# Optimization experiments

Hardware: AMD Instinct MI355X
Metric: run time of the kernel (lower is better)

Reference implementation:

```python
import jax, jax.numpy as jnp
import numpy as np

B, T, D, H = 4, 2048, 1024, 16
DH = D // H
SCALE = 1.0 / np.sqrt(DH)


def setup_inputs() -> dict:
    key = jax.random.key(0)
    ks = jax.random.split(key, 8)
    s = 1.0 / np.sqrt(D)  # keep projections well-scaled
    return {
        "query": jax.random.normal(ks[0], (B, T, D), jnp.float32),
        "key": jax.random.normal(ks[1], (B, T, D), jnp.float32),
        "value": jax.random.normal(ks[2], (B, T, D), jnp.float32),
        "Wq": jax.random.normal(ks[3], (D, D), jnp.float32) * s,
        "bq": jnp.zeros((D,), jnp.float32),
        "Wk": jax.random.normal(ks[4], (D, D), jnp.float32) * s,
        "bk": jnp.zeros((D,), jnp.float32),
        "Wv": jax.random.normal(ks[5], (D, D), jnp.float32) * s,
        "bv": jnp.zeros((D,), jnp.float32),
        "Wo": jax.random.normal(ks[6], (D, D), jnp.float32) * s,
        "bo": jnp.zeros((D,), jnp.float32),
    }


def reference(query, key, value, Wq, bq, Wk, bk, Wv, bv, Wo, bo):
    # Linear projections (torch Linear: x @ W.T + b; W here stored as [out,in])
    Q = query @ Wq.T + bq            # [B,T,D]
    K = key @ Wk.T + bk
    V = value @ Wv.T + bv
    # split heads -> [B,H,T,DH]
    Q = Q.reshape(B, T, H, DH).transpose(0, 2, 1, 3)
    K = K.reshape(B, T, H, DH).transpose(0, 2, 1, 3)
    V = V.reshape(B, T, H, DH).transpose(0, 2, 1, 3)
    # scaled dot-product attention (chunking in the original is a memory
    # optimization, not a math change; no mask, eval-mode dropout = identity)
    scores = jnp.einsum("bhqd,bhkd->bhqk", Q, K) * SCALE
    attn = jax.nn.softmax(scores, axis=-1)
    out = jnp.einsum("bhqk,bhkd->bhqd", attn, V)  # [B,H,T,DH]
    out = out.transpose(0, 2, 1, 3).reshape(B, T, D)
    return out @ Wo.T + bo
```

## Files before the change

### kernel.cpp

```cpp
#include <hip/hip_runtime.h>
#include <hip/hip_bf16.h>

typedef __bf16 bf16x8 __attribute__((ext_vector_type(8)));
typedef float f32x4 __attribute__((ext_vector_type(4)));
typedef float f32x16 __attribute__((ext_vector_type(16)));
typedef unsigned int uint;
typedef unsigned short u16;

#define DEV static __device__ __forceinline__

DEV u16 f2bf(float x) {
    uint u = __builtin_bit_cast(uint, x);
    u += 0x7FFFu + ((u >> 16) & 1u);
    return (u16)(u >> 16);
}

DEV uint cvtpk(float lo, float hi) {
    uint r;
    asm("v_cvt_pk_bf16_f32 %0, %1, %2" : "=v"(r) : "v"(lo), "v"(hi));
    return r;
}

DEV void plswap(uint& a, uint& b) {
    asm("v_permlane32_swap_b32 %0, %1" : "+v"(a), "+v"(b));
}

DEV float fexp2(float x) { return __builtin_amdgcn_exp2f(x); }

DEV void gload16(const void* g, void* l) {
    __builtin_amdgcn_global_load_lds((const __attribute__((address_space(1))) void*)g,
                                     (__attribute__((address_space(3))) void*)l,
                                     16, 0, 0);
}

__global__ __launch_bounds__(256) void k_wconv(const float* __restrict__ w0,
                                               const float* __restrict__ w1,
                                               const float* __restrict__ w2,
                                               const float* __restrict__ w3,
                                               u16* __restrict__ out) {
    const int which = blockIdx.x >> 9;
    const float* in = which == 0 ? w0 : (which == 1 ? w1 : (which == 2 ? w2 : w3));
    const long i = (blockIdx.x & 511) * 256 + threadIdx.x;
    const float4* p = (const float4*)in + i * 2;
    float4 a = p[0], b = p[1];
    uint4 dv;
    dv.x = cvtpk(a.x, a.y); dv.y = cvtpk(a.z, a.w);
    dv.z = cvtpk(b.x, b.y); dv.w = cvtpk(b.z, b.w);
    ((uint4*)(out + ((long)which << 20)))[i] = dv;
}

__global__ __launch_bounds__(256, 2) void k_gemm_qkv(
    const float* __restrict__ Aq, const float* __restrict__ Ak,
    const float* __restrict__ Av, const u16* __restrict__ Bw,
    const float* __restrict__ b0, const float* __restrict__ b1,
    const float* __restrict__ b2, u16* __restrict__ Cb,
    u16* __restrict__ VT) {
    constexpr int N = 1024, K = 1024;
    __shared__ u16 lS[16384];
    u16* lA = lS;
    u16* lB = lS + 8192;
    const int tid = threadIdx.x;
    const int l = tid & 63, w = tid >> 6;
    const int lr = l & 15, lk = l >> 4;
    const int wr = w >> 1, wc = w & 1;
    const int nbn = N >> 7;
    const int cpx = (int)gridDim.x >> 3;
    const int wg = (blockIdx.x & 7) * cpx + (blockIdx.x >> 3);
    const int bm = wg / nbn, bn = wg % nbn;
    const int seg = bm >> 6;
    const float* Aseg = seg == 0 ? Aq : (seg == 1 ? Ak : Av);
    const u16* Bseg = Bw + ((long)seg << 20);
    const float* bias = seg == 0 ? b0 : (seg == 1 ? b1 : b2);
    const int bml = bm & 63;
    const float oscale = seg == 0 ? 0.18033688f : 1.0f;

    const int arow = tid >> 3;
    const int acol = (tid & 7) * 8;
    int adst[4];
    const float* asrc[4];
#pragma unroll
    for (int t = 0; t < 4; ++t) {
        int row = t * 32 + arow;
        adst[t] = row * 128 + ((acol * 2) ^ ((row & 7) << 4));
        asrc[t] = Aseg + (long)(bml * 128 + row) * K + acol;
    }
    long bbase[4];
    int bdst[4];
#pragma unroll
    for (int t = 0; t < 4; ++t) {
        int p = (t * 256 + tid) * 16;
        int row = p >> 7;
        int src = (p & 127) ^ ((row & 7) << 4);
        bdst[t] = p;
        bbase[t] = (long)(bn * 128 + row) * (K * 2) + src;
    }
    const int swz = (lr & 7) << 4;
    int aoff[4][2], boff[4][2];
#pragma unroll
    for (int m = 0; m < 4; ++m)
#pragma unroll
        for (int kc = 0; kc < 2; ++kc) {
            aoff[m][kc] = (wr * 64 + m * 16 + lr) * 128 + ((kc * 64 + lk * 16) ^ swz);
            boff[m][kc] = (wc * 64 + m * 16 + lr) * 128 + ((kc * 64 + lk * 16) ^ swz);
        }

    f32x4 acc[4][4] = {};
    const char* gB = (const char*)Bseg;
    const char* lAb = (const char*)lA;
    const char* lBb = (const char*)lB;
    for (int kt = 0; kt < K / 64; ++kt) {
        __syncthreads();
#pragma unroll
        for (int t = 0; t < 4; ++t)
            gload16(gB + bbase[t] + kt * 128, (char*)lB + bdst[t]);
        float4 f0[4], f1[4];
#pragma unroll
        for (int t = 0; t < 4; ++t) {
            const float* s = asrc[t] + kt * 64;
            f0[t] = *(const float4*)s;
            f1[t] = *(const float4*)(s + 4);
        }
#pragma unroll
        for (int t = 0; t < 4; ++t) {
            uint4 dv;
            dv.x = cvtpk(f0[t].x, f0[t].y);
            dv.y = cvtpk(f0[t].z, f0[t].w);
            dv.z = cvtpk(f1[t].x, f1[t].y);
            dv.w = cvtpk(f1[t].z, f1[t].w);
            *(uint4*)((char*)lA + adst[t]) = dv;
        }
        __syncthreads();
#pragma unroll
        for (int kc = 0; kc < 2; ++kc) {
            bf16x8 av[4], bv[4];
#pragma unroll
            for (int m = 0; m < 4; ++m) av[m] = *(const bf16x8*)(lAb + aoff[m][kc]);
#pragma unroll
            for (int n = 0; n < 4; ++n) bv[n] = *(const bf16x8*)(lBb + boff[n][kc]);
#pragma unroll
            for (int m = 0; m < 4; ++m)
#pragma unroll
                for (int n = 0; n < 4; ++n)
                    acc[m][n] = __builtin_amdgcn_mfma_f32_16x16x32_bf16(av[m], bv[n], acc[m][n], 0, 0, 0);
        }
    }

    const int col0 = bn * 128 + wc * 64;
    float bval[4];
#pragma unroll
    for (int n = 0; n < 4; ++n) bval[n] = bias[col0 + n * 16 + lr];

    if (seg < 2) {
        const int row0 = bm * 128 + wr * 64;
#pragma unroll
        for (int m = 0; m < 4; ++m)
#pragma unroll
            for (int j = 0; j < 4; ++j) {
                int row = row0 + m * 16 + lk * 4 + j;
#pragma unroll
                for (int n = 0; n < 4; ++n)
                    Cb[(long)row * N + col0 + n * 16 + lr] =
                        f2bf((acc[m][n][j] + bval[n]) * oscale);
            }
    } else {
        __syncthreads();
#pragma unroll
        for (int m = 0; m < 4; ++m)
#pragma unroll
            for (int j = 0; j < 4; ++j) {
                int row = wr * 64 + m * 16 + lk * 4 + j;
#pragma unroll
                for (int n = 0; n < 4; ++n) {
                    int col = wc * 64 + n * 16 + lr;
                    *(u16*)((char*)lS + col * 256 + ((row * 2) ^ ((col & 7) << 4))) =
                        f2bf(acc[m][n][j] + bval[n]);
                }
            }
        __syncthreads();
        const int bb = bml >> 4;
        const int t0 = (bml & 15) * 128;
        const int c = tid >> 4;
        const int chunk = tid & 15;
#pragma unroll
        for (int pass = 0; pass < 8; ++pass) {
            int cc = pass * 16 + c;
            uint4 val = *(const uint4*)((const char*)lS + cc * 256 +
                                        ((chunk * 16) ^ ((cc & 7) << 4)));
            int gcol = bn * 128 + cc;
            int hh = gcol >> 6, dh = gcol & 63;
            *(uint4*)((char*)VT +
                      ((((long)(bb * 16 + hh) * 64 + dh) << 11) + t0 + chunk * 8) * 2) = val;
        }
    }
}

__global__ __launch_bounds__(256, 2) void k_gemm_bt(
    const u16* __restrict__ A, const u16* __restrict__ Bw,
    const float* __restrict__ bias, float* __restrict__ Cf,
    int M, int N, int K) {
    __shared__ u16 lA[128 * 64];
    __shared__ u16 lB[128 * 64];
    const int tid = threadIdx.x;
    const int l = tid & 63, w = tid >> 6;
    const int lr = l & 15, lk = l >> 4;
    const int wr = w >> 1, wc = w & 1;
    const int nbn = N >> 7;
    const int cpx = (int)gridDim.x >> 3;
    const int wg = (blockIdx.x & 7) * cpx + (blockIdx.x >> 3);
    const int bm = wg / nbn, bn = wg % nbn;

    long abase[4], bbase[4];
    int ldst[4];
#pragma unroll
    for (int t = 0; t < 4; ++t) {
        int c = t * 256 + tid;
        int p = c * 16;
        int row = p >> 7;
        int inrow = p & 127;
        int src = inrow ^ ((row & 7) << 4);
        ldst[t] = p;
        abase[t] = (long)(bm * 128 + row) * (K * 2) + src;
        bbase[t] = (long)(bn * 128 + row) * (K * 2) + src;
    }
    const int swz = (lr & 7) << 4;
    int aoff[4][2], boff[4][2];
#pragma unroll
    for (int m = 0; m < 4; ++m)
#pragma unroll
        for (int kc = 0; kc < 2; ++kc) {
            aoff[m][kc] = (wr * 64 + m * 16 + lr) * 128 + ((kc * 64 + lk * 16) ^ swz);
            boff[m][kc] = (wc * 64 + m * 16 + lr) * 128 + ((kc * 64 + lk * 16) ^ swz);
        }

    f32x4 acc[4][4] = {};
    const char* gA = (const char*)A;
    const char* gB = (const char*)Bw;
    const char* lAb = (const char*)lA;
    const char* lBb = (const char*)lB;
    const int nkt = K >> 6;
    for (int kt = 0; kt < nkt; ++kt) {
        __syncthreads();
#pragma unroll
        for (int t = 0; t < 4; ++t)
            gload16(gA + abase[t] + kt * 128, (char*)lA + ldst[t]);
#pragma unroll
        for (int t = 0; t < 4; ++t)
            gload16(gB + bbase[t] + kt * 128, (char*)lB + ldst[t]);
        __syncthreads();
#pragma unroll
        for (int kc = 0; kc < 2; ++kc) {
            bf16x8 av[4], bv[4];
#pragma unroll
            for (int m = 0; m < 4; ++m) av[m] = *(const bf16x8*)(lAb + aoff[m][kc]);
#pragma unroll
            for (int n = 0; n < 4; ++n) bv[n] = *(const bf16x8*)(lBb + boff[n][kc]);
#pragma unroll
            for (int m = 0; m < 4; ++m)
#pragma unroll
                for (int n = 0; n < 4; ++n)
                    acc[m][n] = __builtin_amdgcn_mfma_f32_16x16x32_bf16(av[m], bv[n], acc[m][n], 0, 0, 0);
        }
    }

    const int row0 = bm * 128 + wr * 64;
    const int col0 = bn * 128 + wc * 64;
    float bval[4];
#pragma unroll
    for (int n = 0; n < 4; ++n) bval[n] = bias[col0 + n * 16 + lr];
#pragma unroll
    for (int m = 0; m < 4; ++m)
#pragma unroll
        for (int j = 0; j < 4; ++j) {
            int row = row0 + m * 16 + lk * 4 + j;
#pragma unroll
            for (int n = 0; n < 4; ++n)
                Cf[(long)row * N + col0 + n * 16 + lr] = acc[m][n][j] + bval[n];
        }
}

__global__ __launch_bounds__(512, 4) void k_attn6(
    const u16* __restrict__ Qb, const u16* __restrict__ Kb,
    const u16* __restrict__ VTb, u16* __restrict__ Ob) {
    constexpr int T = 2048, D = 1024;
    constexpr int NT = T / 64;
    __shared__ u16 sK[2][4096];
    __shared__ u16 sV[2][4096];
    const int tid = threadIdx.x;
    const int l = tid & 63, w = tid >> 6;
    const int hi = l >> 5;
    const int q32 = l & 31;
    const int hi16 = hi * 16;
    const int kswz = (q32 & 7) << 4;
    const int bid = blockIdx.x;
    const int bh = (bid & 7) * 8 + ((bid >> 3) & 7);
    const int qt = bid >> 6;
    const int b = bh >> 4, h = bh & 15;

    const char* Qg = (const char*)(Qb + (long)b * T * D + h * 64);
    const char* Kg = (const char*)(Kb + (long)b * T * D + h * 64);
    const char* VTg = (const char*)(VTb + (long)bh * 64 * 2048);
    const int q0 = qt * 256 + w * 32;

    bf16x8 qf[4];
#pragma unroll
    for (int c = 0; c < 4; ++c)
        qf[c] = *(const bf16x8*)(Qg + (long)(q0 + q32) * 2048 + c * 32 + hi16);

    const int srow = tid >> 3;
    const int ssrc = ((tid & 7) * 16) ^ ((srow & 7) << 4);
    const int sdst = tid * 16;
    const long kbase = (long)srow * 2048 + ssrc;
    const long vbase = (long)srow * 4096 + ssrc;

    union { u16 s[8]; bf16x8 v; } ones_u;
#pragma unroll
    for (int i = 0; i < 8; ++i) ones_u.s[i] = 0x3F80;
    const bf16x8 onesv = ones_u.v;

#define STAGE(kt_, buf_) do {                                                  \
        gload16(Kg + (long)(kt_) * 64 * 2048 + kbase, (char*)sK[buf_] + sdst); \
        gload16(VTg + (kt_) * 128 + vbase, (char*)sV[buf_] + sdst);            \
    } while (0)

    STAGE(0, 0);
    __syncthreads();

    f32x16 o[2] = {};
    f32x16 lacc = {};

    for (int kt = 0; kt < NT; ++kt) {
        if (kt + 1 < NT) STAGE(kt + 1, (kt + 1) & 1);

        const char* kbp = (const char*)sK[kt & 1];
        f32x16 st[2] = {};
        __builtin_amdgcn_s_setprio(1);
#pragma unroll
        for (int c = 0; c < 4; ++c) {
            bf16x8 kf = *(const bf16x8*)(kbp + q32 * 128 + ((c * 32 + hi16) ^ kswz));
            st[0] = __builtin_amdgcn_mfma_f32_32x32x16_bf16(kf, qf[c], st[0], 0, 0, 0);
        }
#pragma unroll
        for (int c = 0; c < 4; ++c) {
            bf16x8 kf = *(const bf16x8*)(kbp + (32 + q32) * 128 + ((c * 32 + hi16) ^ kswz));
            st[1] = __builtin_amdgcn_mfma_f32_32x32x16_bf16(kf, qf[c], st[1], 0, 0, 0);
        }
        __builtin_amdgcn_s_setprio(0);

#pragma unroll
        for (int n = 0; n < 2; ++n)
#pragma unroll
            for (int r = 0; r < 16; ++r)
                st[n][r] = fexp2(st[n][r]);

        const char* vbp = (const char*)sV[kt & 1];
        __builtin_amdgcn_s_setprio(1);
#pragma unroll
        for (int c = 0; c < 4; ++c) {
            const int n = c >> 1, rb = (c & 1) * 8;
            uint A0 = cvtpk(st[n][rb + 0], st[n][rb + 1]);
            uint A1 = cvtpk(st[n][rb + 2], st[n][rb + 3]);
            uint B0 = cvtpk(st[n][rb + 4], st[n][rb + 5]);
            uint B1 = cvtpk(st[n][rb + 6], st[n][rb + 7]);
            plswap(A0, B0);
            plswap(A1, B1);
            union { uint u[4]; bf16x8 v; } pa;
            pa.u[0] = A0; pa.u[1] = A1; pa.u[2] = B0; pa.u[3] = B1;
            int cb = c * 32 + hi16;
            bf16x8 v0 = *(const bf16x8*)(vbp + q32 * 128 + (cb ^ kswz));
            bf16x8 v1 = *(const bf16x8*)(vbp + (32 + q32) * 128 + (cb ^ kswz));
            o[0] = __builtin_amdgcn_mfma_f32_32x32x16_bf16(pa.v, v0, o[0], 0, 0, 0);
            o[1] = __builtin_amdgcn_mfma_f32_32x32x16_bf16(pa.v, v1, o[1], 0, 0, 0);
            lacc  = __builtin_amdgcn_mfma_f32_32x32x16_bf16(pa.v, onesv, lacc, 0, 0, 0);
        }
        __builtin_amdgcn_s_setprio(0);
        __syncthreads();
    }
#undef STAGE

#pragma unroll
    for (int r = 0; r < 16; ++r) {
        float inv = 1.f / lacc[r];
        int srcq = (r & 3) + 8 * (r >> 2) + 4 * hi;
        int trow = q0 + srcq;
        char* orow = (char*)Ob + ((long)(b * T + trow) * D + h * 64) * 2;
        *(u16*)(orow + q32 * 2) = f2bf(o[0][r] * inv);
        *(u16*)(orow + (32 + q32) * 2) = f2bf(o[1][r] * inv);
    }
}

extern "C" void kernel_launch(void* const* d_in, const int* in_sizes, int n_in,
                              void* d_out, int out_size, void* d_ws, size_t ws_size,
                              hipStream_t stream) {
    const float* q  = (const float*)d_in[0];
    const float* k  = (const float*)d_in[1];
    const float* v  = (const float*)d_in[2];
    const float* Wq = (const float*)d_in[3];
    const float* bq = (const float*)d_in[4];
    const float* Wk = (const float*)d_in[5];
    const float* bk = (const float*)d_in[6];
    const float* Wv = (const float*)d_in[7];
    const float* bv = (const float*)d_in[8];
    const float* Wo = (const float*)d_in[9];
    const float* bo = (const float*)d_in[10];

    const long MT = 8192L * 1024;
    const long WT = 1024L * 1024;
    u16* ws   = (u16*)d_ws;
    u16* wall = ws;
    u16* qbf  = wall + 4 * WT;
    u16* kbf  = qbf + MT;
    u16* vtb  = kbf + MT;
    u16* abf  = vtb + MT;

    k_wconv<<<dim3(2048), dim3(256), 0, stream>>>(Wq, Wk, Wv, Wo, wall);

    k_gemm_qkv<<<dim3(1536), dim3(256), 0, stream>>>(q, k, v, wall,
                                                     bq, bk, bv, qbf, vtb);

    k_attn6<<<dim3(512), dim3(512), 0, stream>>>(qbf, kbf, vtb, abf);

    k_gemm_bt<<<dim3(512), dim3(256), 0, stream>>>(abf, wall + 3 * WT, bo,
                                                   (float*)d_out, 8192, 1024, 1024);
}
```

Baseline: 188.2 us.

## Compute softmax row sums on VALU and stage 128-key tiles per iteration

The attention kernel now loads 128 keys and values per pipeline stage instead of 64 and processes them as two halves. This halves the number of barriers and stage issues per block. The softmax denominator is no longer accumulated with an extra MFMA against a ones vector; instead each lane sums its exponentials in fp32 registers and combines them across lanes with shuffles. This removes a third of the PV-phase MFMAs, but doubles shared memory per block (64 KB), which may reduce how many blocks fit per CU.

```diff
diff --git a/kernel.cpp b/kernel.cpp
--- a/kernel.cpp
+++ b/kernel.cpp
@@ -278,13 +278,13 @@
         }
 }
 
-__global__ __launch_bounds__(512, 4) void k_attn6(
+__global__ __launch_bounds__(512, 4) void k_attn7(
     const u16* __restrict__ Qb, const u16* __restrict__ Kb,
     const u16* __restrict__ VTb, u16* __restrict__ Ob) {
     constexpr int T = 2048, D = 1024;
-    constexpr int NT = T / 64;
-    __shared__ u16 sK[2][4096];
-    __shared__ u16 sV[2][4096];
+    constexpr int NT2 = T / 128;
+    __shared__ u16 sK[2][8192];
+    __shared__ u16 sV[2][8192];
     const int tid = threadIdx.x;
     const int l = tid & 63, w = tid >> 6;
     const int hi = l >> 5;
@@ -306,81 +306,97 @@
     for (int c = 0; c < 4; ++c)
         qf[c] = *(const bf16x8*)(Qg + (long)(q0 + q32) * 2048 + c * 32 + hi16);
 
-    const int srow = tid >> 3;
-    const int ssrc = ((tid & 7) * 16) ^ ((srow & 7) << 4);
-    const int sdst = tid * 16;
-    const long kbase = (long)srow * 2048 + ssrc;
-    const long vbase = (long)srow * 4096 + ssrc;
-
-    union { u16 s[8]; bf16x8 v; } ones_u;
-#pragma unroll
-    for (int i = 0; i < 8; ++i) ones_u.s[i] = 0x3F80;
-    const bf16x8 onesv = ones_u.v;
-
-#define STAGE(kt_, buf_) do {                                                  \
-        gload16(Kg + (long)(kt_) * 64 * 2048 + kbase, (char*)sK[buf_] + sdst); \
-        gload16(VTg + (kt_) * 128 + vbase, (char*)sV[buf_] + sdst);            \
+    long kbase[2], vbase[2];
+    int sdst[2];
+#pragma unroll
+    for (int t = 0; t < 2; ++t) {
+        int id = tid + t * 512;
+        sdst[t] = id * 16;
+        int kr = id >> 3, kp = (id & 7) * 16;
+        kbase[t] = (long)kr * 2048 + (kp ^ ((kr & 7) << 4));
+        int vr = id >> 4, vp = (id & 15) * 16;
+        vbase[t] = (long)vr * 4096 + (vp ^ ((vr & 7) << 4));
+    }
+
+#define STAGE2(kt_, buf_) do {                                                  \
+        long kb = (long)(kt_) * 128 * 2048;                                     \
+        gload16(Kg + kb + kbase[0], (char*)sK[buf_] + sdst[0]);                 \
+        gload16(Kg + kb + kbase[1], (char*)sK[buf_] + sdst[1]);                 \
+        gload16(VTg + (kt_) * 256 + vbase[0], (char*)sV[buf_] + sdst[0]);       \
+        gload16(VTg + (kt_) * 256 + vbase[1], (char*)sV[buf_] + sdst[1]);       \
     } while (0)
 
-    STAGE(0, 0);
+    STAGE2(0, 0);
     __syncthreads();
 
     f32x16 o[2] = {};
-    f32x16 lacc = {};
-
-    for (int kt = 0; kt < NT; ++kt) {
-        if (kt + 1 < NT) STAGE(kt + 1, (kt + 1) & 1);
+    float ls0 = 0.f, ls1 = 0.f, ls2 = 0.f, ls3 = 0.f;
+
+    for (int kt = 0; kt < NT2; ++kt) {
+        if (kt + 1 < NT2) STAGE2(kt + 1, (kt + 1) & 1);
 
         const char* kbp = (const char*)sK[kt & 1];
-        f32x16 st[2] = {};
-        __builtin_amdgcn_s_setprio(1);
-#pragma unroll
-        for (int c = 0; c < 4; ++c) {
-            bf16x8 kf = *(const bf16x8*)(kbp + q32 * 128 + ((c * 32 + hi16) ^ kswz));
-            st[0] = __builtin_amdgcn_mfma_f32_32x32x16_bf16(kf, qf[c], st[0], 0, 0, 0);
-        }
-#pragma unroll
-        for (int c = 0; c < 4; ++c) {
-            bf16x8 kf = *(const bf16x8*)(kbp + (32 + q32) * 128 + ((c * 32 + hi16) ^ kswz));
-            st[1] = __builtin_amdgcn_mfma_f32_32x32x16_bf16(kf, qf[c], st[1], 0, 0, 0);
-        }
-        __builtin_amdgcn_s_setprio(0);
-
-#pragma unroll
-        for (int n = 0; n < 2; ++n)
-#pragma unroll
-            for (int r = 0; r < 16; ++r)
-                st[n][r] = fexp2(st[n][r]);
-
         const char* vbp = (const char*)sV[kt & 1];
-        __builtin_amdgcn_s_setprio(1);
-#pragma unroll
-        for (int c = 0; c < 4; ++c) {
-            const int n = c >> 1, rb = (c & 1) * 8;
-            uint A0 = cvtpk(st[n][rb + 0], st[n][rb + 1]);
-            uint A1 = cvtpk(st[n][rb + 2], st[n][rb + 3]);
-            uint B0 = cvtpk(st[n][rb + 4], st[n][rb + 5]);
-            uint B1 = cvtpk(st[n][rb + 6], st[n][rb + 7]);
-            plswap(A0, B0);
-            plswap(A1, B1);
-            union { uint u[4]; bf16x8 v; } pa;
-            pa.u[0] = A0; pa.u[1] = A1; pa.u[2] = B0; pa.u[3] = B1;
-            int cb = c * 32 + hi16;
-            bf16x8 v0 = *(const bf16x8*)(vbp + q32 * 128 + (cb ^ kswz));
-            bf16x8 v1 = *(const bf16x8*)(vbp + (32 + q32) * 128 + (cb ^ kswz));
-            o[0] = __builtin_amdgcn_mfma_f32_32x32x16_bf16(pa.v, v0, o[0], 0, 0, 0);
-            o[1] = __builtin_amdgcn_mfma_f32_32x32x16_bf16(pa.v, v1, o[1], 0, 0, 0);
-            lacc  = __builtin_amdgcn_mfma_f32_32x32x16_bf16(pa.v, onesv, lacc, 0, 0, 0);
-        }
-        __builtin_amdgcn_s_setprio(0);
-        __syncthreads();
-    }
-#undef STAGE
-
+#pragma unroll
+        for (int half = 0; half < 2; ++half) {
+            f32x16 st[2] = {};
+            __builtin_amdgcn_s_setprio(1);
+#pragma unroll
+            for (int c = 0; c < 4; ++c) {
+                bf16x8 kf = *(const bf16x8*)(kbp + (half * 64 + q32) * 128 +
+                                             ((c * 32 + hi16) ^ kswz));
+                st[0] = __builtin_amdgcn_mfma_f32_32x32x16_bf16(kf, qf[c], st[0], 0, 0, 0);
+            }
+#pragma unroll
+            for (int c = 0; c < 4; ++c) {
+                bf16x8 kf = *(const bf16x8*)(kbp + (half * 64 + 32 + q32) * 128 +
+                                             ((c * 32 + hi16) ^ kswz));
+                st[1] = __builtin_amdgcn_mfma_f32_32x32x16_bf16(kf, qf[c], st[1], 0, 0, 0);
+            }
+            __builtin_amdgcn_s_setprio(0);
+
+#pragma unroll
+            for (int n = 0; n < 2; ++n)
+#pragma unroll
+                for (int r = 0; r < 16; ++r) {
+                    float p = fexp2(st[n][r]);
+                    st[n][r] = p;
+                    if ((r & 3) == 0) ls0 += p;
+                    else if ((r & 3) == 1) ls1 += p;
+                    else if ((r & 3) == 2) ls2 += p;
+                    else ls3 += p;
+                }
+
+            __builtin_amdgcn_s_setprio(1);
+#pragma unroll
+            for (int c = 0; c < 4; ++c) {
+                const int n = c >> 1, rb = (c & 1) * 8;
+                uint A0 = cvtpk(st[n][rb + 0], st[n][rb + 1]);
+                uint A1 = cvtpk(st[n][rb + 2], st[n][rb + 3]);
+                uint B0 = cvtpk(st[n][rb + 4], st[n][rb + 5]);
+                uint B1 = cvtpk(st[n][rb + 6], st[n][rb + 7]);
+                plswap(A0, B0);
+                plswap(A1, B1);
+                union { uint u[4]; bf16x8 v; } pa;
+                pa.u[0] = A0; pa.u[1] = A1; pa.u[2] = B0; pa.u[3] = B1;
+                int cb = (c * 32 + hi16) ^ kswz;
+                bf16x8 v0 = *(const bf16x8*)(vbp + q32 * 256 + half * 128 + cb);
+                bf16x8 v1 = *(const bf16x8*)(vbp + (32 + q32) * 256 + half * 128 + cb);
+                o[0] = __builtin_amdgcn_mfma_f32_32x32x16_bf16(pa.v, v0, o[0], 0, 0, 0);
+                o[1] = __builtin_amdgcn_mfma_f32_32x32x16_bf16(pa.v, v1, o[1], 0, 0, 0);
+            }
+            __builtin_amdgcn_s_setprio(0);
+        }
+        __syncthreads();
+    }
+#undef STAGE2
+
+    float lsum = (ls0 + ls1) + (ls2 + ls3);
+    float total = lsum + __shfl_xor(lsum, 32);
 #pragma unroll
     for (int r = 0; r < 16; ++r) {
-        float inv = 1.f / lacc[r];
         int srcq = (r & 3) + 8 * (r >> 2) + 4 * hi;
+        float inv = 1.f / __shfl(total, srcq);
         int trow = q0 + srcq;
         char* orow = (char*)Ob + ((long)(b * T + trow) * D + h * 64) * 2;
         *(u16*)(orow + q32 * 2) = f2bf(o[0][r] * inv);
@@ -417,7 +433,7 @@
     k_gemm_qkv<<<dim3(1536), dim3(256), 0, stream>>>(q, k, v, wall,
                                                      bq, bk, bv, qbf, vtb);
 
-    k_attn6<<<dim3(512), dim3(512), 0, stream>>>(qbf, kbf, vtb, abf);
+    k_attn7<<<dim3(512), dim3(512), 0, stream>>>(qbf, kbf, vtb, abf);
 
     k_gemm_bt<<<dim3(512), dim3(256), 0, stream>>>(abf, wall + 3 * WT, bo,
                                                    (float*)d_out, 8192, 1024, 1024);
```

Measured after the change: 185.8 us. About the same (-1.3%).
